# Performance work log

Hardware: AMD Instinct MI355X
Metric: run time of the kernel (lower is better)

The kernel has to match this reference:

```python
import jax, jax.numpy as jnp
import numpy as np

INPUT_SIZE = 2048
HIDDEN_SIZE = 2048
BATCH = 4096


def setup_inputs() -> dict:
    key = jax.random.key(0)
    ks = jax.random.split(key, 12)
    std = 1.0 / HIDDEN_SIZE ** 0.5
    def u(k, shape):
        return jax.random.uniform(k, shape, jnp.float32, -std, std)
    inp = {
        "x": jax.random.normal(ks[0], (BATCH, INPUT_SIZE), jnp.float32),
        "h": jax.random.normal(ks[1], (BATCH, HIDDEN_SIZE), jnp.float32),
        "c": jax.random.normal(ks[2], (BATCH, HIDDEN_SIZE), jnp.float32),
        "weight_ii": u(ks[3], (HIDDEN_SIZE, INPUT_SIZE)),
        "weight_if": u(ks[4], (HIDDEN_SIZE, INPUT_SIZE)),
        "weight_ig": u(ks[5], (HIDDEN_SIZE, INPUT_SIZE)),
        "weight_io": u(ks[6], (HIDDEN_SIZE, INPUT_SIZE)),
        "weight_hi": u(ks[7], (HIDDEN_SIZE, HIDDEN_SIZE)),
        "weight_hf": u(ks[8], (HIDDEN_SIZE, HIDDEN_SIZE)),
        "weight_hg": u(ks[9], (HIDDEN_SIZE, HIDDEN_SIZE)),
        "weight_ho": u(ks[10], (HIDDEN_SIZE, HIDDEN_SIZE)),
        "bias_i": u(ks[11], (HIDDEN_SIZE,)),
        "bias_f": u(jax.random.fold_in(key, 100), (HIDDEN_SIZE,)),
        "bias_g": u(jax.random.fold_in(key, 101), (HIDDEN_SIZE,)),
        "bias_o": u(jax.random.fold_in(key, 102), (HIDDEN_SIZE,)),
    }
    return inp


def reference(x, h, c, weight_ii, weight_if, weight_ig, weight_io,
              weight_hi, weight_hf, weight_hg, weight_ho,
              bias_i, bias_f, bias_g, bias_o):
    # Fuse the 4 input projections and 4 hidden projections into 2 GEMMs
    # (same math as 8 separate matmuls in the original module).
    W_x = jnp.concatenate([weight_ii, weight_if, weight_ig, weight_io], axis=0)  # [4H, I]
    W_h = jnp.concatenate([weight_hi, weight_hf, weight_hg, weight_ho], axis=0)  # [4H, H]
    b = jnp.concatenate([bias_i, bias_f, bias_g, bias_o], axis=0)                # [4H]
    gates = x @ W_x.T + h @ W_h.T + b                                            # [B, 4H]
    gi, gf, gg, go = jnp.split(gates, 4, axis=1)
    i = jax.nn.sigmoid(gi)
    f = jax.nn.sigmoid(gf)
    g = jnp.tanh(gg)
    o = jax.nn.sigmoid(go)
    c_new = f * c + i * g
    h_new = o * jnp.tanh(c_new)
    return (h_new, c_new)
```

## Files before the change

kernel.cpp:

```cpp
#include <hip/hip_runtime.h>
#include <cstdint>
#include <cstddef>

#define BATCH 4096
#define HID   2048

typedef __attribute__((ext_vector_type(8))) short bf16x8;
typedef __attribute__((ext_vector_type(4))) float f32x4;

__device__ __forceinline__ unsigned short f2bf(float f) {
  union { float f; unsigned u; } a; a.f = f;
  unsigned u = a.u;
  return (unsigned short)((u + 0x7FFFu + ((u >> 16) & 1u)) >> 16);
}

__device__ __forceinline__ void gload_lds16(const void* g, void* l) {
  __builtin_amdgcn_global_load_lds((const __attribute__((address_space(1))) void*)g,
                                   (__attribute__((address_space(3))) void*)l, 16, 0, 0);
}

#define SCHED0() __builtin_amdgcn_sched_barrier(0)
#define SBAR()  do { SCHED0(); __builtin_amdgcn_s_barrier(); SCHED0(); } while (0)
#define WAITV(N) do { SCHED0(); asm volatile("s_waitcnt vmcnt(" #N ")" ::: "memory"); SCHED0(); } while (0)
#define WAITL(N) do { SCHED0(); asm volatile("s_waitcnt lgkmcnt(" #N ")" ::: "memory"); SCHED0(); } while (0)
#define DSR(dst, adr, IMM) asm volatile("ds_read_b128 %0, %1 offset:" #IMM : "=v"(dst) : "v"(adr))
#define PRIO1() __builtin_amdgcn_s_setprio(1)
#define PRIO0() __builtin_amdgcn_s_setprio(0)

#define READ_CLUSTER(AADR, BADR) do { \
  DSR(a1[0], (AADR), 0); DSR(a1[1], (AADR), 1024); DSR(a1[2], (AADR), 2048); DSR(a1[3], (AADR), 3072); \
  DSR(bf_[0], (BADR), 0); DSR(bf_[1], (BADR), 1024); DSR(bf_[2], (BADR), 2048); DSR(bf_[3], (BADR), 3072); \
  DSR(a2[0], (AADR), 4096); DSR(a2[1], (AADR), 5120); DSR(a2[2], (AADR), 6144); DSR(a2[3], (AADR), 7168); \
} while (0)

#define MFMA_HALF(AF, OFS) do { \
  _Pragma("unroll") \
  for (int m_ = 0; m_ < 4; m_++) { \
    _Pragma("unroll") \
    for (int n_ = 0; n_ < 4; n_++) \
      acc[(OFS) + m_][n_] = __builtin_amdgcn_mfma_f32_16x16x32_bf16(AF[m_], bf_[n_], acc[(OFS) + m_][n_], 0, 0, 0); \
  } \
} while (0)

#define STAGE_G(KOFF, DOF) do { \
  gload_lds16(pA + (KOFF), dA + (DOF)); \
  gload_lds16(pA + 128 * 4096 + (KOFF), dA + (DOF) + 8192); \
  gload_lds16(pB + (KOFF), dA + (DOF) + 16384); \
  gload_lds16(pB + 32 * 4096 + (KOFF), dA + (DOF) + 24576); } while (0)

#define ADV2(o) do { (o) += 65536; if ((o) >= 163840) (o) -= 163840; } while (0)

#define INTERVAL(STG1, STG2) do { \
  WAITV(0); \
  SBAR(); \
  READ_CLUSTER(aB0 + (unsigned)o_a, bB0 + (unsigned)o_a); \
  STG1; \
  WAITL(0); \
  PRIO1(); MFMA_HALF(a1, 0); MFMA_HALF(a2, 4); PRIO0(); \
  READ_CLUSTER(aB0 + (unsigned)o_b, bB0 + (unsigned)o_b); \
  STG2; \
  WAITL(0); \
  PRIO1(); MFMA_HALF(a1, 0); MFMA_HALF(a2, 4); PRIO0(); \
  ADV2(o_a); ADV2(o_b); ADV2(o_s1); ADV2(o_s2); ks += 64; \
} while (0)

__global__ __launch_bounds__(256) void convert_kernel(
    const float* __restrict__ x, const float* __restrict__ h,
    const float* __restrict__ wii, const float* __restrict__ wif,
    const float* __restrict__ wig, const float* __restrict__ wio,
    const float* __restrict__ whi, const float* __restrict__ whf,
    const float* __restrict__ whg, const float* __restrict__ who,
    unsigned short* __restrict__ Abf, unsigned short* __restrict__ Wbf) {
  int seg = blockIdx.y;
  const float* src;
  unsigned short* dst;
  int ofs;
  size_t rofs;
  if (seg < 4) {
    src = (seg < 2) ? x : h;
    dst = Abf;
    ofs = (seg < 2) ? 0 : 2048;
    rofs = (seg & 1) ? 2048 : 0;
    src += rofs * 2048;
  } else {
    int g = (seg - 4) & 3;
    dst = Wbf + (size_t)g * 2048 * 4096;
    ofs = (seg >= 8) ? 2048 : 0;
    rofs = 0;
    switch (seg) {
      case 4: src = wii; break; case 5: src = wif; break;
      case 6: src = wig; break; case 7: src = wio; break;
      case 8: src = whi; break; case 9: src = whf; break;
      case 10: src = whg; break; default: src = who; break;
    }
  }
  size_t idx = (size_t)blockIdx.x * 256 + threadIdx.x;
  size_t e = idx * 4;
  int n = (int)(e >> 11);
  int k = (int)(e & 2047);
  float4 v = *(const float4*)(src + e);
  ushort4 o;
  o.x = f2bf(v.x); o.y = f2bf(v.y); o.z = f2bf(v.z); o.w = f2bf(v.w);
  *(ushort4*)(dst + (rofs + (size_t)n) * 4096 + ofs + k) = o;
}

__global__ __launch_bounds__(512, 2) void lstm_gemm8(
    const unsigned short* __restrict__ Abf, const unsigned short* __restrict__ Wbf,
    const float* __restrict__ c_in,
    const float* __restrict__ bias_i, const float* __restrict__ bias_f,
    const float* __restrict__ bias_g, const float* __restrict__ bias_o,
    float* __restrict__ out) {
  __shared__ unsigned short lds[5 * 16384];

  int tid = threadIdx.x;
  int lane = tid & 63;
  int wid = tid >> 6;
  int wr = wid >> 2;
  int wc = wid & 3;
  int lrow = lane & 15;
  int qh = lane >> 4;

  int bid = blockIdx.x;
  int xcd = bid & 7;
  int t7 = bid >> 3;
  int mt = t7 & 15;
  int bn = xcd * 4 + (t7 >> 4);
  int m0 = mt * 256;

  int r0 = tid >> 2, cc0 = tid & 3;
  int ccs0 = cc0 ^ ((r0 >> 1) & 3);
  const unsigned short* pA = Abf + (size_t)(m0 + r0) * 4096 + ccs0 * 8;
  int g0 = (r0 >> 4) & 3;
  int jw = bn * 64 + ((r0 >> 6) & 3) * 16 + (r0 & 15);
  const unsigned short* pB = Wbf + ((size_t)g0 * 2048 + jw) * 4096 + ccs0 * 8;

  char* L0 = (char*)&lds[0];
  char* dA = L0 + tid * 16;
  unsigned ldsOff = (unsigned)(size_t)(__attribute__((address_space(3))) char*)L0;

  int arow0 = wr * 128 + lrow;
  int brow0 = wc * 64 + lrow;
  unsigned qsA = ((unsigned)(qh ^ ((arow0 >> 1) & 3))) << 4;
  unsigned qsB = ((unsigned)(qh ^ ((brow0 >> 1) & 3))) << 4;
  unsigned aB0 = ldsOff + (unsigned)arow0 * 64 + qsA;
  unsigned bB0 = ldsOff + 16384u + (unsigned)brow0 * 64 + qsB;

  f32x4 acc[8][4];
  #pragma unroll
  for (int a = 0; a < 8; a++)
    #pragma unroll
    for (int b = 0; b < 4; b++) acc[a][b] = (f32x4){0.f, 0.f, 0.f, 0.f};

  bf16x8 a1[4], a2[4], bf_[4];

  int o_a = 0, o_b = 32768, o_s1 = 65536, o_s2 = 98304;
  int ks = 64;

  STAGE_G(0, 0);
  STAGE_G(32, 32768);

  for (int t = 0; t < 63; ++t) {
    INTERVAL(STAGE_G(ks, o_s1), STAGE_G(ks + 32, o_s2));
  }
  INTERVAL((void)0, (void)0);

  int j = bn * 64 + wc * 16 + lrow;
  float bi = bias_i[j], bff = bias_f[j], bgg = bias_g[j], bo = bias_o[j];
  int rbase = m0 + wr * 128 + qh * 4;
  #pragma unroll
  for (int mf = 0; mf < 8; mf++) {
    #pragma unroll
    for (int qq = 0; qq < 4; qq++) {
      int m = rbase + mf * 16 + qq;
      size_t off = (size_t)m * HID + j;
      float gi = acc[mf][0][qq] + bi;
      float gf = acc[mf][1][qq] + bff;
      float gg = acc[mf][2][qq] + bgg;
      float go = acc[mf][3][qq] + bo;
      float iv = 1.f / (1.f + __expf(-gi));
      float fv = 1.f / (1.f + __expf(-gf));
      float gv = tanhf(gg);
      float ov = 1.f / (1.f + __expf(-go));
      float cn = fv * c_in[off] + iv * gv;
      float hn = ov * tanhf(cn);
      out[off] = hn;
      out[(size_t)BATCH * HID + off] = cn;
    }
  }
}

__global__ __launch_bounds__(256) void lstm_gemm_fb(
    const float* __restrict__ x, const float* __restrict__ h,
    const float* __restrict__ wii, const float* __restrict__ wif,
    const float* __restrict__ wig, const float* __restrict__ wio,
    const float* __restrict__ whi, const float* __restrict__ whf,
    const float* __restrict__ whg, const float* __restrict__ who,
    const float* __restrict__ c_in,
    const float* __restrict__ bias_i, const float* __restrict__ bias_f,
    const float* __restrict__ bias_g, const float* __restrict__ bias_o,
    float* __restrict__ out) {
  __shared__ unsigned short Ald[128 * 64];
  __shared__ unsigned short Bld[128 * 64];
  int tid = threadIdx.x;
  int lane = tid & 63;
  int wid = tid >> 6;
  int wr = wid >> 1, wc = wid & 1;
  int bid = blockIdx.x;
  int swz = (bid & 7) * 256 + (bid >> 3);
  int mt = swz & 31;
  int ht = swz >> 5;
  int m0 = mt * 128;
  int j0 = ht * 32;
  f32x4 acc[4][4];
  #pragma unroll
  for (int a = 0; a < 4; a++)
    #pragma unroll
    for (int b = 0; b < 4; b++) acc[a][b] = (f32x4){0.f, 0.f, 0.f, 0.f};
  int lrow = lane & 15;
  int lsw = lrow & 7;
  int qbase = lane >> 4;
  for (int kt = 0; kt < 64; kt++) {
    int k0 = kt * 64;
    const float* Asrc = (k0 < 2048) ? x : h;
    int ka = k0 & 2047;
    #pragma unroll
    for (int i = 0; i < 4; i++) {
      int c = i * 256 + tid;
      int r = c >> 3, cc = c & 7;
      int ccs = cc ^ (r & 7);
      const float* s = Asrc + (size_t)(m0 + r) * 2048 + ka + ccs * 8;
      float4 v0 = *(const float4*)s;
      float4 v1 = *(const float4*)(s + 4);
      bf16x8 pk;
      pk[0] = (short)f2bf(v0.x); pk[1] = (short)f2bf(v0.y);
      pk[2] = (short)f2bf(v0.z); pk[3] = (short)f2bf(v0.w);
      pk[4] = (short)f2bf(v1.x); pk[5] = (short)f2bf(v1.y);
      pk[6] = (short)f2bf(v1.z); pk[7] = (short)f2bf(v1.w);
      *(bf16x8*)((char*)Ald + (size_t)c * 16) = pk;
    }
    #pragma unroll
    for (int i = 0; i < 4; i++) {
      int c = i * 256 + tid;
      int rb = c >> 3, cc = c & 7;
      int ccs = cc ^ (rb & 7);
      int g = rb >> 5, jj = rb & 31;
      const float* Bsrc;
      if (k0 < 2048) Bsrc = (g == 0) ? wii : (g == 1) ? wif : (g == 2) ? wig : wio;
      else           Bsrc = (g == 0) ? whi : (g == 1) ? whf : (g == 2) ? whg : who;
      const float* s = Bsrc + (size_t)(j0 + jj) * 2048 + ka + ccs * 8;
      float4 v0 = *(const float4*)s;
      float4 v1 = *(const float4*)(s + 4);
      bf16x8 pk;
      pk[0] = (short)f2bf(v0.x); pk[1] = (short)f2bf(v0.y);
      pk[2] = (short)f2bf(v0.z); pk[3] = (short)f2bf(v0.w);
      pk[4] = (short)f2bf(v1.x); pk[5] = (short)f2bf(v1.y);
      pk[6] = (short)f2bf(v1.z); pk[7] = (short)f2bf(v1.w);
      *(bf16x8*)((char*)Bld + (size_t)c * 16) = pk;
    }
    __syncthreads();
    #pragma unroll
    for (int ks = 0; ks < 2; ks++) {
      int q = ks * 4 + qbase;
      int qs8 = (q ^ lsw) * 8;
      bf16x8 af[4], bg[4];
      #pragma unroll
      for (int mf = 0; mf < 4; mf++)
        af[mf] = *(const bf16x8*)&Ald[(wr * 64 + mf * 16 + lrow) * 64 + qs8];
      #pragma unroll
      for (int g = 0; g < 4; g++)
        bg[g] = *(const bf16x8*)&Bld[(g * 32 + wc * 16 + lrow) * 64 + qs8];
      #pragma unroll
      for (int mf = 0; mf < 4; mf++)
        #pragma unroll
        for (int g = 0; g < 4; g++)
          acc[mf][g] = __builtin_amdgcn_mfma_f32_16x16x32_bf16(af[mf], bg[g], acc[mf][g], 0, 0, 0);
    }
    __syncthreads();
  }
  int j = j0 + wc * 16 + lrow;
  float bi = bias_i[j], bff = bias_f[j], bgg = bias_g[j], bo = bias_o[j];
  int rbase = m0 + wr * 64 + (lane >> 4) * 4;
  #pragma unroll
  for (int mf = 0; mf < 4; mf++) {
    #pragma unroll
    for (int q = 0; q < 4; q++) {
      int m = rbase + mf * 16 + q;
      size_t off = (size_t)m * HID + j;
      float gi = acc[mf][0][q] + bi;
      float gf = acc[mf][1][q] + bff;
      float gg = acc[mf][2][q] + bgg;
      float go = acc[mf][3][q] + bo;
      float iv = 1.f / (1.f + __expf(-gi));
      float fv = 1.f / (1.f + __expf(-gf));
      float gv = tanhf(gg);
      float ov = 1.f / (1.f + __expf(-go));
      float cn = fv * c_in[off] + iv * gv;
      float hn = ov * tanhf(cn);
      out[off] = hn;
      out[(size_t)BATCH * HID + off] = cn;
    }
  }
}

extern "C" void kernel_launch(void* const* d_in, const int* in_sizes, int n_in,
                              void* d_out, int out_size, void* d_ws, size_t ws_size,
                              hipStream_t stream) {
  const float* x   = (const float*)d_in[0];
  const float* h   = (const float*)d_in[1];
  const float* c   = (const float*)d_in[2];
  const float* wii = (const float*)d_in[3];
  const float* wif = (const float*)d_in[4];
  const float* wig = (const float*)d_in[5];
  const float* wio = (const float*)d_in[6];
  const float* whi = (const float*)d_in[7];
  const float* whf = (const float*)d_in[8];
  const float* whg = (const float*)d_in[9];
  const float* who = (const float*)d_in[10];
  const float* bi  = (const float*)d_in[11];
  const float* bf  = (const float*)d_in[12];
  const float* bg  = (const float*)d_in[13];
  const float* bo  = (const float*)d_in[14];
  float* out = (float*)d_out;

  size_t needA = (size_t)4096 * 4096 * 2;
  size_t needW = (size_t)8192 * 4096 * 2;

  if (ws_size >= needA + needW) {
    unsigned short* Abf = (unsigned short*)d_ws;
    unsigned short* Wbf = (unsigned short*)((char*)d_ws + needA);
    convert_kernel<<<dim3(4096, 12), 256, 0, stream>>>(
        x, h, wii, wif, wig, wio, whi, whf, whg, who, Abf, Wbf);
    lstm_gemm8<<<512, 512, 0, stream>>>(Abf, Wbf, c, bi, bf, bg, bo, out);
  } else {
    lstm_gemm_fb<<<2048, 256, 0, stream>>>(
        x, h, wii, wif, wig, wio, whi, whf, whg, who,
        c, bi, bf, bg, bo, out);
  }
}
```

Measured before the change: 318.7 us.

## Replace 8-wave 256x256 GEMM tile with 4-wave 256x128 double-buffered tile

```diff
diff --git a/kernel.cpp b/kernel.cpp
--- a/kernel.cpp
+++ b/kernel.cpp
@@ -42,26 +42,13 @@
   } \
 } while (0)
 
-#define STAGE_G(KOFF, DOF) do { \
-  gload_lds16(pA + (KOFF), dA + (DOF)); \
-  gload_lds16(pA + 128 * 4096 + (KOFF), dA + (DOF) + 8192); \
-  gload_lds16(pB + (KOFF), dA + (DOF) + 16384); \
-  gload_lds16(pB + 32 * 4096 + (KOFF), dA + (DOF) + 24576); } while (0)
-
-#define ADV2(o) do { (o) += 65536; if ((o) >= 163840) (o) -= 163840; } while (0)
-
-#define INTERVAL(STG1, STG2) do { \
-  WAITV(0); \
-  SBAR(); \
-  READ_CLUSTER(aB0 + (unsigned)o_a, bB0 + (unsigned)o_a); \
-  STG1; \
-  WAITL(0); \
-  PRIO1(); MFMA_HALF(a1, 0); MFMA_HALF(a2, 4); PRIO0(); \
-  READ_CLUSTER(aB0 + (unsigned)o_b, bB0 + (unsigned)o_b); \
-  STG2; \
-  WAITL(0); \
-  PRIO1(); MFMA_HALF(a1, 0); MFMA_HALF(a2, 4); PRIO0(); \
-  ADV2(o_a); ADV2(o_b); ADV2(o_s1); ADV2(o_s2); ks += 64; \
+#define STAGE6(KOFF, DOF) do { \
+  gload_lds16(pA + (KOFF),          dD + (DOF)); \
+  gload_lds16(pA + 262144 + (KOFF), dD + (DOF) + 4096); \
+  gload_lds16(pA + 524288 + (KOFF), dD + (DOF) + 8192); \
+  gload_lds16(pA + 786432 + (KOFF), dD + (DOF) + 12288); \
+  gload_lds16(pB + (KOFF),          dD + (DOF) + 16384); \
+  gload_lds16(pB + 65536 + (KOFF),  dD + (DOF) + 20480); \
 } while (0)
 
 __global__ __launch_bounds__(256) void convert_kernel(
@@ -104,19 +91,19 @@
   *(ushort4*)(dst + (rofs + (size_t)n) * 4096 + ofs + k) = o;
 }
 
-__global__ __launch_bounds__(512, 2) void lstm_gemm8(
+__global__ __launch_bounds__(256, 2) void lstm_gemm2(
     const unsigned short* __restrict__ Abf, const unsigned short* __restrict__ Wbf,
     const float* __restrict__ c_in,
     const float* __restrict__ bias_i, const float* __restrict__ bias_f,
     const float* __restrict__ bias_g, const float* __restrict__ bias_o,
     float* __restrict__ out) {
-  __shared__ unsigned short lds[5 * 16384];
+  __shared__ unsigned short lds[2 * 12288];
 
   int tid = threadIdx.x;
   int lane = tid & 63;
   int wid = tid >> 6;
-  int wr = wid >> 2;
-  int wc = wid & 3;
+  int wr = wid >> 1;
+  int wc = wid & 1;
   int lrow = lane & 15;
   int qh = lane >> 4;
 
@@ -124,26 +111,22 @@
   int xcd = bid & 7;
   int t7 = bid >> 3;
   int mt = t7 & 15;
-  int bn = xcd * 4 + (t7 >> 4);
+  int bn = xcd * 8 + (t7 >> 4);
   int m0 = mt * 256;
 
   int r0 = tid >> 2, cc0 = tid & 3;
   int ccs0 = cc0 ^ ((r0 >> 1) & 3);
   const unsigned short* pA = Abf + (size_t)(m0 + r0) * 4096 + ccs0 * 8;
   int g0 = (r0 >> 4) & 3;
-  int jw = bn * 64 + ((r0 >> 6) & 3) * 16 + (r0 & 15);
-  const unsigned short* pB = Wbf + ((size_t)g0 * 2048 + jw) * 4096 + ccs0 * 8;
+  const unsigned short* pB = Wbf + ((size_t)g0 * 2048 + bn * 32 + (r0 & 15)) * 4096 + ccs0 * 8;
 
   char* L0 = (char*)&lds[0];
-  char* dA = L0 + tid * 16;
+  char* dD = L0 + tid * 16;
   unsigned ldsOff = (unsigned)(size_t)(__attribute__((address_space(3))) char*)L0;
 
-  int arow0 = wr * 128 + lrow;
-  int brow0 = wc * 64 + lrow;
-  unsigned qsA = ((unsigned)(qh ^ ((arow0 >> 1) & 3))) << 4;
-  unsigned qsB = ((unsigned)(qh ^ ((brow0 >> 1) & 3))) << 4;
-  unsigned aB0 = ldsOff + (unsigned)arow0 * 64 + qsA;
-  unsigned bB0 = ldsOff + 16384u + (unsigned)brow0 * 64 + qsB;
+  unsigned qs = ((unsigned)(qh ^ ((lrow >> 1) & 3))) << 4;
+  unsigned aB0 = ldsOff + (unsigned)(wr * 128 + lrow) * 64 + qs;
+  unsigned bB0 = ldsOff + 16384u + (unsigned)(wc * 64 + lrow) * 64 + qs;
 
   f32x4 acc[8][4];
   #pragma unroll
@@ -153,18 +136,30 @@
 
   bf16x8 a1[4], a2[4], bf_[4];
 
-  int o_a = 0, o_b = 32768, o_s1 = 65536, o_s2 = 98304;
-  int ks = 64;
-
-  STAGE_G(0, 0);
-  STAGE_G(32, 32768);
-
-  for (int t = 0; t < 63; ++t) {
-    INTERVAL(STAGE_G(ks, o_s1), STAGE_G(ks + 32, o_s2));
-  }
-  INTERVAL((void)0, (void)0);
-
-  int j = bn * 64 + wc * 16 + lrow;
+  STAGE6(0, 0);
+  unsigned o = 0;
+
+  for (int c = 0; c < 127; ++c) {
+    WAITV(0);
+    SBAR();
+    READ_CLUSTER(aB0 + o, bB0 + o);
+    unsigned os = o ^ 24576u;
+    STAGE6((c + 1) * 32, os);
+    WAITL(4);
+    PRIO1(); MFMA_HALF(a1, 0); PRIO0();
+    WAITL(0);
+    PRIO1(); MFMA_HALF(a2, 4); PRIO0();
+    o = os;
+  }
+  WAITV(0);
+  SBAR();
+  READ_CLUSTER(aB0 + o, bB0 + o);
+  WAITL(4);
+  PRIO1(); MFMA_HALF(a1, 0); PRIO0();
+  WAITL(0);
+  PRIO1(); MFMA_HALF(a2, 4); PRIO0();
+
+  int j = bn * 32 + wc * 16 + lrow;
   float bi = bias_i[j], bff = bias_f[j], bgg = bias_g[j], bo = bias_o[j];
   int rbase = m0 + wr * 128 + qh * 4;
   #pragma unroll
@@ -330,7 +325,7 @@
     unsigned short* Wbf = (unsigned short*)((char*)d_ws + needA);
     convert_kernel<<<dim3(4096, 12), 256, 0, stream>>>(
         x, h, wii, wif, wig, wio, whi, whf, whg, who, Abf, Wbf);
-    lstm_gemm8<<<512, 512, 0, stream>>>(Abf, Wbf, c, bi, bf, bg, bo, out);
+    lstm_gemm2<<<1024, 256, 0, stream>>>(Abf, Wbf, c, bi, bf, bg, bo, out);
   } else {
     lstm_gemm_fb<<<2048, 256, 0, stream>>>(
         x, h, wii, wif, wig, wio, whi, whf, whg, who,
```

New measurement: 346.7 us. 1.09x slower.
